# Kernel optimization log

Hardware: AMD Instinct MI355X
Metric: run time of the kernel (lower is better)

## Reference

```python
import jax, jax.numpy as jnp
import numpy as np

EPS = 1e-6
NUM_HEADS = 16
CAPACITY_FACTOR = 0.5


def _layernorm(x, g, b):
    mu = jnp.mean(x, axis=-1, keepdims=True)
    var = jnp.mean((x - mu) ** 2, axis=-1, keepdims=True)
    return (x - mu) * jax.lax.rsqrt(var + EPS) * g + b


def setup_inputs() -> dict:
    key = jax.random.key(0)
    ks = jax.random.split(key, 12)
    B, S, H, F = 2, 2048, 1024, 4096
    s = lambda d: 1.0 / np.sqrt(d)
    return {
        "x": jax.random.normal(ks[0], (B, S, H), jnp.float32),
        "w_router": jax.random.normal(ks[1], (1, H), jnp.float32) * s(H),
        "ln1_g": jnp.ones((H,), jnp.float32),
        "ln1_b": jnp.zeros((H,), jnp.float32),
        "wq": jax.random.normal(ks[2], (H, H), jnp.float32) * s(H),
        "wk": jax.random.normal(ks[3], (H, H), jnp.float32) * s(H),
        "wv": jax.random.normal(ks[4], (H, H), jnp.float32) * s(H),
        "wo": jax.random.normal(ks[5], (H, H), jnp.float32) * s(H),
        "ln2_g": jnp.ones((H,), jnp.float32),
        "ln2_b": jnp.zeros((H,), jnp.float32),
        "w_gate": jax.random.normal(ks[6], (F, H), jnp.float32) * s(H),
        "w_up": jax.random.normal(ks[7], (F, H), jnp.float32) * s(H),
        "w_down": jax.random.normal(ks[8], (H, F), jnp.float32) * s(F),
    }


def reference(x, w_router, ln1_g, ln1_b, wq, wk, wv, wo, ln2_g, ln2_b, w_gate, w_up, w_down):
    B, S, H = x.shape
    nh = NUM_HEADS
    hd = H // nh
    scale = hd ** -0.5

    # --- TokenRouter (training path, straight-through) ---
    router_logits = jnp.einsum("bsh,oh->bso", x, w_router)[..., 0]  # [B,S]
    capacity = int(S * CAPACITY_FACTOR)
    _, top_idx = jax.lax.top_k(router_logits, capacity)  # [B,cap]
    routing_mask = jnp.zeros((B, S), x.dtype).at[jnp.arange(B)[:, None], top_idx].set(1.0)
    probs = jax.nn.sigmoid(router_logits)
    routing_weights = (routing_mask + probs - jax.lax.stop_gradient(probs))[..., None]  # [B,S,1]

    # --- Attention sub-block ---
    residual = x
    xn = _layernorm(x, ln1_g, ln1_b)
    q = jnp.einsum("bsh,oh->bso", xn, wq).reshape(B, S, nh, hd).transpose(0, 2, 1, 3)
    k = jnp.einsum("bsh,oh->bso", xn, wk).reshape(B, S, nh, hd).transpose(0, 2, 1, 3)
    v = jnp.einsum("bsh,oh->bso", xn, wv).reshape(B, S, nh, hd).transpose(0, 2, 1, 3)
    scores = jnp.einsum("bnqd,bnkd->bnqk", q, k) * scale
    causal = jnp.triu(jnp.full((S, S), -jnp.inf, x.dtype), k=1)
    attn = jax.nn.softmax(scores + causal, axis=-1)
    out = jnp.einsum("bnqk,bnkd->bnqd", attn, v).transpose(0, 2, 1, 3).reshape(B, S, H)
    attn_out = jnp.einsum("bsh,oh->bso", out, wo)
    x = residual + routing_weights * attn_out

    # --- FFN sub-block (SwiGLU) ---
    residual = x
    xn = _layernorm(x, ln2_g, ln2_b)
    gate = jax.nn.silu(jnp.einsum("bsh,fh->bsf", xn, w_gate))
    up = jnp.einsum("bsh,fh->bsf", xn, w_up)
    ffn_out = jnp.einsum("bsf,hf->bsh", gate * up, w_down)
    x = residual + routing_weights * ffn_out

    return x, router_logits
```

## Files before the change

### kernel.cpp

```cpp
#include <hip/hip_runtime.h>
#include <hip/hip_bf16.h>

typedef unsigned short u16;
typedef __attribute__((ext_vector_type(4))) float f32x4;
typedef __attribute__((ext_vector_type(8))) short short8;
typedef __attribute__((ext_vector_type(4))) unsigned short ushort4v;

#define LOG2E 1.4426950408889634f

__device__ __forceinline__ u16 f2bfu(float f) {
  unsigned int u = __float_as_uint(f);
  u += 0x7FFFu + ((u >> 16) & 1u);
  return (u16)(u >> 16);
}
__device__ __forceinline__ f32x4 mfma16(short8 a, short8 b, f32x4 c) {
  return __builtin_amdgcn_mfma_f32_16x16x32_bf16(a, b, c, 0, 0, 0);
}
__device__ __forceinline__ void gld16(const void* g, void* l) {
  __builtin_amdgcn_global_load_lds(
      (const __attribute__((address_space(1))) void*)g,
      (__attribute__((address_space(3))) void*)l, 16, 0, 0);
}
template <int CTRL>
__device__ __forceinline__ float dppf(float x) {
  int xi = __float_as_int(x);
  return __int_as_float(__builtin_amdgcn_update_dpp(xi, xi, CTRL, 0xf, 0xf, false));
}
__device__ __forceinline__ float rsum16(float v) {
  v += dppf<0x121>(v);
  v += dppf<0x122>(v);
  v += dppf<0x124>(v);
  v += dppf<0x128>(v);
  return v;
}

__global__ void k_cvt7(const float* __restrict__ s0, const float* __restrict__ s1,
                       const float* __restrict__ s2, const float* __restrict__ s3,
                       const float* __restrict__ s4, const float* __restrict__ s5,
                       const float* __restrict__ s6,
                       u16* __restrict__ d0, u16* __restrict__ d1, u16* __restrict__ d2,
                       u16* __restrict__ d3, u16* __restrict__ d4, u16* __restrict__ d5,
                       u16* __restrict__ d6) {
  const int y = blockIdx.y;
  const float* src; u16* dst; int n4;
  switch (y) {
    case 0: src = s0; dst = d0; n4 = 262144; break;
    case 1: src = s1; dst = d1; n4 = 262144; break;
    case 2: src = s2; dst = d2; n4 = 262144; break;
    case 3: src = s3; dst = d3; n4 = 262144; break;
    case 4: src = s4; dst = d4; n4 = 1048576; break;
    case 5: src = s5; dst = d5; n4 = 1048576; break;
    default: src = s6; dst = d6; n4 = 1048576; break;
  }
  int i = blockIdx.x * blockDim.x + threadIdx.x;
  if (i < n4) {
    float4 v = ((const float4*)src)[i];
    ushort4v o;
    o.x = f2bfu(v.x); o.y = f2bfu(v.y); o.z = f2bfu(v.z); o.w = f2bfu(v.w);
    *(ushort4v*)(dst + (size_t)i * 4) = o;
  }
}

__global__ void k_router_ln(const float* __restrict__ x, const float* __restrict__ wr,
                            const float* __restrict__ g, const float* __restrict__ bb,
                            float* __restrict__ logits, float* __restrict__ out_lg,
                            float* __restrict__ out_x, u16* __restrict__ xn) {
  int t = blockIdx.x * 4 + (threadIdx.x >> 6);
  int l = threadIdx.x & 63;
  const float* xp = x + (size_t)t * 1024;
  float* op = out_x + (size_t)t * 1024;
  float4 xv[4];
  float s = 0.f, sq = 0.f, lg = 0.f;
#pragma unroll
  for (int p = 0; p < 4; ++p) {
    xv[p] = *(const float4*)(xp + (p * 64 + l) * 4);
    float4 wv = *(const float4*)(wr + (p * 64 + l) * 4);
    lg += xv[p].x * wv.x + xv[p].y * wv.y + xv[p].z * wv.z + xv[p].w * wv.w;
    s += xv[p].x + xv[p].y + xv[p].z + xv[p].w;
    sq += xv[p].x * xv[p].x + xv[p].y * xv[p].y + xv[p].z * xv[p].z + xv[p].w * xv[p].w;
    *(float4*)(op + (p * 64 + l) * 4) = xv[p];
  }
#pragma unroll
  for (int off = 32; off; off >>= 1) {
    lg += __shfl_xor(lg, off);
    s += __shfl_xor(s, off);
    sq += __shfl_xor(sq, off);
  }
  float mu = s * (1.f / 1024.f);
  float var = sq * (1.f / 1024.f) - mu * mu;
  float rs = rsqrtf(var + 1e-6f);
#pragma unroll
  for (int p = 0; p < 4; ++p) {
    float4 gv = *(const float4*)(g + (p * 64 + l) * 4);
    float4 bv = *(const float4*)(bb + (p * 64 + l) * 4);
    ushort4v o;
    o.x = f2bfu((xv[p].x - mu) * rs * gv.x + bv.x);
    o.y = f2bfu((xv[p].y - mu) * rs * gv.y + bv.y);
    o.z = f2bfu((xv[p].z - mu) * rs * gv.z + bv.z);
    o.w = f2bfu((xv[p].w - mu) * rs * gv.w + bv.w);
    *(ushort4v*)(xn + (size_t)t * 1024 + (p * 64 + l) * 4) = o;
  }
  if (l == 0) { logits[t] = lg; out_lg[t] = lg; }
}

__global__ void k_mask(const float* __restrict__ logits, float* __restrict__ mask) {
  __shared__ float lg[2048];
  int b = blockIdx.y;
  const float* lp = logits + b * 2048;
  for (int j = threadIdx.x; j < 2048; j += 256) lg[j] = lp[j];
  __syncthreads();
  int t = threadIdx.x >> 2, qtr = threadIdx.x & 3;
  int i = blockIdx.x * 64 + t;
  float my = lg[i];
  int cnt = 0;
  for (int j = qtr * 512; j < qtr * 512 + 512; j += 4) {
    float4 v = *(const float4*)&lg[j];
    cnt += (v.x > my) || (v.x == my && (j + 0) < i);
    cnt += (v.y > my) || (v.y == my && (j + 1) < i);
    cnt += (v.z > my) || (v.z == my && (j + 2) < i);
    cnt += (v.w > my) || (v.w == my && (j + 3) < i);
  }
  cnt += __shfl_xor(cnt, 1);
  cnt += __shfl_xor(cnt, 2);
  if (qtr == 0) mask[b * 2048 + i] = (cnt < 1024) ? 1.0f : 0.0f;
}

__global__ void k_scan(const float* __restrict__ mask, int* __restrict__ idx) {
  __shared__ int wsum[4];
  int b = blockIdx.x;
  const float* mp = mask + b * 2048;
  int t = threadIdx.x, lane = t & 63, wv = t >> 6;
  int sel[8]; int c = 0;
#pragma unroll
  for (int j = 0; j < 8; ++j) { sel[j] = mp[t * 8 + j] > 0.5f; c += sel[j]; }
  int sc = c;
#pragma unroll
  for (int off = 1; off < 64; off <<= 1) {
    int u = __shfl_up(sc, off);
    if (lane >= off) sc += u;
  }
  if (lane == 63) wsum[wv] = sc;
  __syncthreads();
  int woff = 0;
  for (int i = 0; i < wv; ++i) woff += wsum[i];
  int pos = woff + sc - c;
#pragma unroll
  for (int j = 0; j < 8; ++j)
    if (sel[j]) idx[b * 1024 + pos++] = t * 8 + j;
}

__global__ void k_vtrans(const u16* __restrict__ V, u16* __restrict__ VT) {
  int bh = blockIdx.y;
  int b = bh >> 4, h = bh & 15;
  int w = threadIdx.x >> 6, l = threadIdx.x & 63;
  int s0 = (blockIdx.x * 4 + w) * 32;
  const u16* vb = V + ((size_t)b * 2048) * 1024 + h * 64 + l;
  u16 vals[32];
#pragma unroll
  for (int j = 0; j < 32; ++j) vals[j] = vb[(size_t)(s0 + j) * 1024];
  u16* ob = VT + ((size_t)bh * 64 + l) * 2048 + s0;
#pragma unroll
  for (int c = 0; c < 4; ++c) {
    short8 o;
#pragma unroll
    for (int j = 0; j < 8; ++j) o[j] = (short)vals[c * 8 + j];
    *(short8*)&ob[c * 8] = o;
  }
}

__device__ __forceinline__ void gemm_core64(
    const u16* __restrict__ A, const u16* __restrict__ W,
    u16 (&Al)[2][128][64], u16 (&Bl)[2][128][64],
    int m0, int n0, int K, int k0, int nsteps, f32x4 (&acc)[4][4]) {
  const int tid = threadIdx.x, w = tid >> 6, l = tid & 63;
  const int wr = (w >> 1) * 64, wc = (w & 1) * 64;
#pragma unroll
  for (int mt = 0; mt < 4; ++mt)
#pragma unroll
    for (int nt = 0; nt < 4; ++nt) acc[mt][nt] = (f32x4){0.f, 0.f, 0.f, 0.f};

  auto stage = [&](int bf, int t) {
#pragma unroll
    for (int i = 0; i < 4; ++i) {
      const int bc = (i * 4 + w) * 64;
      const int chunk = bc + l;
      const int row = chunk >> 3, cc = chunk & 7;
      gld16(A + (size_t)(m0 + row) * K + k0 + t * 64 + cc * 8, (char*)(&Al[bf][0][0]) + bc * 16);
      gld16(W + (size_t)(n0 + row) * K + k0 + t * 64 + cc * 8, (char*)(&Bl[bf][0][0]) + bc * 16);
    }
  };

  stage(0, 0);
  for (int t = 0; t < nsteps; ++t) {
    __syncthreads();
    if (t + 1 < nsteps) stage((t + 1) & 1, t + 1);
    const int bf = t & 1;
#pragma unroll
    for (int kk = 0; kk < 2; ++kk) {
      const int ko = kk * 32 + (l >> 4) * 8;
      short8 af[4], bv[4];
#pragma unroll
      for (int mt = 0; mt < 4; ++mt) af[mt] = *(const short8*)&Al[bf][wr + mt * 16 + (l & 15)][ko];
#pragma unroll
      for (int nt = 0; nt < 4; ++nt) bv[nt] = *(const short8*)&Bl[bf][wc + nt * 16 + (l & 15)][ko];
#pragma unroll
      for (int mt = 0; mt < 4; ++mt)
#pragma unroll
        for (int nt = 0; nt < 4; ++nt)
          acc[mt][nt] = mfma16(af[mt], bv[nt], acc[mt][nt]);
    }
  }
}

__global__ __launch_bounds__(256, 3)
void k_qkv2(const u16* __restrict__ A, const int* __restrict__ idx,
            const u16* __restrict__ Wq, const u16* __restrict__ Wk, const u16* __restrict__ Wv,
            u16* __restrict__ Qc, u16* __restrict__ Ko, u16* __restrict__ Vo) {
  __shared__ alignas(16) u16 Al[2][128][32];
  __shared__ alignas(16) u16 Bl[2][128][32];
  const int tid = threadIdx.x, w = tid >> 6, l = tid & 63;
  const int b = blockIdx.x, xcd = b & 7, j = b >> 3;
  const u16* W; u16* Ot; int m0, n0; bool isQ;
  if (j < 16) {
    isQ = true;
    int rowg = (xcd >> 1) * 4 + (j >> 2);
    int col  = (xcd & 1) * 4 + (j & 3);
    m0 = rowg * 128; n0 = col * 128; W = Wq; Ot = Qc;
  } else {
    isQ = false;
    int jj = j - 16;
    int rowg = (xcd >> 1) * 8 + (jj >> 3);
    int colg = (xcd & 1) * 8 + (jj & 7);
    m0 = rowg * 128; n0 = (colg & 7) * 128;
    W = (colg >> 3) ? Wv : Wk; Ot = (colg >> 3) ? Vo : Ko;
  }
  int srow[2];
#pragma unroll
  for (int i = 0; i < 2; ++i) {
    int r = (i * 256 + tid) >> 2;
    int row = m0 + r;
    if (isQ) {
      int b2 = row >> 10;
      srow[i] = b2 * 2048 + idx[b2 * 1024 + (row & 1023)];
    } else srow[i] = row;
  }
  const int wr = (w >> 1) * 64, wc = (w & 1) * 64;
  f32x4 acc[4][4];
#pragma unroll
  for (int mt = 0; mt < 4; ++mt)
#pragma unroll
    for (int nt = 0; nt < 4; ++nt) acc[mt][nt] = (f32x4){0.f, 0.f, 0.f, 0.f};

  auto stage = [&](int bf, int t) {
#pragma unroll
    for (int i = 0; i < 2; ++i) {
      const int c = i * 256 + tid;
      const int r = c >> 2, cc = c & 3;
      gld16(A + (size_t)srow[i] * 1024 + t * 32 + cc * 8, (char*)(&Al[bf][0][0]) + c * 16);
      gld16(W + (size_t)(n0 + r) * 1024 + t * 32 + cc * 8, (char*)(&Bl[bf][0][0]) + c * 16);
    }
  };

  stage(0, 0);
  for (int t = 0; t < 32; ++t) {
    __syncthreads();
    if (t + 1 < 32) stage((t + 1) & 1, t + 1);
    const int bf = t & 1;
    const int ko = (l >> 4) * 8;
    short8 af[4], bv[4];
#pragma unroll
    for (int mt = 0; mt < 4; ++mt) af[mt] = *(const short8*)&Al[bf][wr + mt * 16 + (l & 15)][ko];
#pragma unroll
    for (int nt = 0; nt < 4; ++nt) bv[nt] = *(const short8*)&Bl[bf][wc + nt * 16 + (l & 15)][ko];
#pragma unroll
    for (int mt = 0; mt < 4; ++mt)
#pragma unroll
      for (int nt = 0; nt < 4; ++nt)
        acc[mt][nt] = mfma16(af[mt], bv[nt], acc[mt][nt]);
  }
#pragma unroll
  for (int mt = 0; mt < 4; ++mt)
#pragma unroll
    for (int nt = 0; nt < 4; ++nt) {
      int row = m0 + wr + mt * 16 + ((l >> 4) << 2);
      int colo = n0 + wc + nt * 16 + (l & 15);
#pragma unroll
      for (int r = 0; r < 4; ++r)
        Ot[(size_t)(row + r) * 1024 + colo] = f2bfu(acc[mt][nt][r]);
    }
}

__global__ __launch_bounds__(256, 2)
void k_projsk(const u16* __restrict__ A, const u16* __restrict__ W,
              float* __restrict__ P0, float* __restrict__ P1,
              float* __restrict__ P2, float* __restrict__ P3,
              int K, int slice) {
  __shared__ alignas(16) u16 Al[2][128][64];
  __shared__ alignas(16) u16 Bl[2][128][64];
  const int b = blockIdx.x, xcd = b & 7, k = b >> 3;
  const int pair = xcd * 8 + (k >> 3);
  const int rowg = pair >> 2, z = pair & 3, col = k & 7;
  const int n0 = col * 128, m0 = rowg * 128, k0 = z * slice;
  float* P = z == 0 ? P0 : (z == 1 ? P1 : (z == 2 ? P2 : P3));
  f32x4 acc[4][4];
  gemm_core64(A, W, Al, Bl, m0, n0, K, k0, slice >> 6, acc);
  const int tid = threadIdx.x, w = tid >> 6, l = tid & 63;
  const int wr = (w >> 1) * 64, wc = (w & 1) * 64;
#pragma unroll
  for (int mt = 0; mt < 4; ++mt)
#pragma unroll
    for (int nt = 0; nt < 4; ++nt) {
      int row = m0 + wr + mt * 16 + ((l >> 4) << 2);
      int colo = n0 + wc + nt * 16 + (l & 15);
#pragma unroll
      for (int r = 0; r < 4; ++r)
        P[(size_t)(row + r) * 1024 + colo] = acc[mt][nt][r];
    }
}

__global__ void k_combine(const float* __restrict__ P0, const float* __restrict__ P1,
                          const float* __restrict__ P2, const float* __restrict__ P3,
                          const int* __restrict__ idx, const float* __restrict__ resid,
                          float* __restrict__ out) {
  int slot = blockIdx.x * 2 + (threadIdx.x >> 7);
  int c0 = (threadIdx.x & 127) * 8;
  int b = slot >> 10;
  int orig = idx[b * 1024 + (slot & 1023)];
  size_t po = (size_t)slot * 1024 + c0;
  size_t go = ((size_t)(b * 2048 + orig)) * 1024 + c0;
#pragma unroll
  for (int h = 0; h < 2; ++h) {
    float4 a = *(const float4*)(P0 + po + h * 4);
    float4 bb = *(const float4*)(P1 + po + h * 4);
    float4 c = *(const float4*)(P2 + po + h * 4);
    float4 d = *(const float4*)(P3 + po + h * 4);
    float4 rr = *(const float4*)(resid + go + h * 4);
    float4 o;
    o.x = rr.x + a.x + bb.x + c.x + d.x;
    o.y = rr.y + a.y + bb.y + c.y + d.y;
    o.z = rr.z + a.z + bb.z + c.z + d.z;
    o.w = rr.w + a.w + bb.w + c.w + d.w;
    *(float4*)(out + go + h * 4) = o;
  }
}

__global__ void k_combine_ln(const float* __restrict__ P0, const float* __restrict__ P1,
                             const float* __restrict__ P2, const float* __restrict__ P3,
                             const int* __restrict__ idx, const float* __restrict__ resid,
                             const float* __restrict__ g, const float* __restrict__ bb,
                             float* __restrict__ out, u16* __restrict__ xn2) {
  __shared__ float red[2][2][2];
  int sh = threadIdx.x >> 7;
  int slot = blockIdx.x * 2 + sh;
  int tl = threadIdx.x & 127;
  int c0 = tl * 8;
  int b = slot >> 10;
  int orig = idx[b * 1024 + (slot & 1023)];
  size_t po = (size_t)slot * 1024 + c0;
  size_t go = ((size_t)(b * 2048 + orig)) * 1024 + c0;
  float v[8];
  float s = 0.f, sq = 0.f;
#pragma unroll
  for (int h = 0; h < 2; ++h) {
    float4 a = *(const float4*)(P0 + po + h * 4);
    float4 b4 = *(const float4*)(P1 + po + h * 4);
    float4 c = *(const float4*)(P2 + po + h * 4);
    float4 d = *(const float4*)(P3 + po + h * 4);
    float4 rr = *(const float4*)(resid + go + h * 4);
    float4 o;
    o.x = rr.x + a.x + b4.x + c.x + d.x;
    o.y = rr.y + a.y + b4.y + c.y + d.y;
    o.z = rr.z + a.z + b4.z + c.z + d.z;
    o.w = rr.w + a.w + b4.w + c.w + d.w;
    *(float4*)(out + go + h * 4) = o;
    v[h * 4 + 0] = o.x; v[h * 4 + 1] = o.y; v[h * 4 + 2] = o.z; v[h * 4 + 3] = o.w;
    s += o.x + o.y + o.z + o.w;
    sq += o.x * o.x + o.y * o.y + o.z * o.z + o.w * o.w;
  }
#pragma unroll
  for (int off = 32; off; off >>= 1) { s += __shfl_xor(s, off); sq += __shfl_xor(sq, off); }
  if ((tl & 63) == 0) { red[sh][tl >> 6][0] = s; red[sh][tl >> 6][1] = sq; }
  __syncthreads();
  float ts = red[sh][0][0] + red[sh][1][0];
  float tsq = red[sh][0][1] + red[sh][1][1];
  float mu = ts * (1.f / 1024.f);
  float var = tsq * (1.f / 1024.f) - mu * mu;
  float rs = rsqrtf(var + 1e-6f);
#pragma unroll
  for (int h = 0; h < 2; ++h) {
    float4 gv = *(const float4*)(g + c0 + h * 4);
    float4 bv = *(const float4*)(bb + c0 + h * 4);
    ushort4v o;
    o.x = f2bfu((v[h * 4 + 0] - mu) * rs * gv.x + bv.x);
    o.y = f2bfu((v[h * 4 + 1] - mu) * rs * gv.y + bv.y);
    o.z = f2bfu((v[h * 4 + 2] - mu) * rs * gv.z + bv.z);
    o.w = f2bfu((v[h * 4 + 3] - mu) * rs * gv.w + bv.w);
    *(ushort4v*)(xn2 + (size_t)slot * 1024 + c0 + h * 4) = o;
  }
}

__global__ __launch_bounds__(256, 2)
void k_ffn_dual(const u16* __restrict__ A, const u16* __restrict__ Wg, const u16* __restrict__ Wu,
                u16* __restrict__ H, int N, int K) {
  __shared__ alignas(16) u16 Al[2][128][32];
  __shared__ alignas(16) u16 Bgl[2][128][32];
  __shared__ alignas(16) u16 Bul[2][128][32];
  const int tid = threadIdx.x, w = tid >> 6, l = tid & 63;
  const int b = blockIdx.x, xcd = b & 7, k = b >> 3;
  const int rowg = (xcd >> 2) * 8 + (k >> 3);
  const int col  = (xcd & 3) * 8 + (k & 7);
  const int n0 = col * 128, m0 = rowg * 128;
  const int wr = (w >> 1) * 64, wc = (w & 1) * 64;
  f32x4 ag[4][4], au[4][4];
#pragma unroll
  for (int mt = 0; mt < 4; ++mt)
#pragma unroll
    for (int nt = 0; nt < 4; ++nt) {
      ag[mt][nt] = (f32x4){0.f, 0.f, 0.f, 0.f};
      au[mt][nt] = (f32x4){0.f, 0.f, 0.f, 0.f};
    }
  const int nsteps = K >> 5;

  auto stage = [&](int bf, int t) {
#pragma unroll
    for (int i = 0; i < 2; ++i) {
      const int bc = (i * 4 + w) * 64;
      const int chunk = bc + l;
      const int row = chunk >> 2, cc = chunk & 3;
      const size_t ao = (size_t)(m0 + row) * K + t * 32 + cc * 8;
      const size_t bo = (size_t)(n0 + row) * K + t * 32 + cc * 8;
      gld16(A + ao,  (char*)(&Al[bf][0][0])  + bc * 16);
      gld16(Wg + bo, (char*)(&Bgl[bf][0][0]) + bc * 16);
      gld16(Wu + bo, (char*)(&Bul[bf][0][0]) + bc * 16);
    }
  };

  stage(0, 0);
  for (int t = 0; t < nsteps; ++t) {
    __syncthreads();
    if (t + 1 < nsteps) stage((t + 1) & 1, t + 1);
    const int bf = t & 1;
    const int ko = (l >> 4) * 8;
    short8 af[4], bg[4], bu[4];
#pragma unroll
    for (int mt = 0; mt < 4; ++mt) af[mt] = *(const short8*)&Al[bf][wr + mt * 16 + (l & 15)][ko];
#pragma unroll
    for (int nt = 0; nt < 4; ++nt) {
      bg[nt] = *(const short8*)&Bgl[bf][wc + nt * 16 + (l & 15)][ko];
      bu[nt] = *(const short8*)&Bul[bf][wc + nt * 16 + (l & 15)][ko];
    }
#pragma unroll
    for (int mt = 0; mt < 4; ++mt)
#pragma unroll
      for (int nt = 0; nt < 4; ++nt) {
        ag[mt][nt] = mfma16(af[mt], bg[nt], ag[mt][nt]);
        au[mt][nt] = mfma16(af[mt], bu[nt], au[mt][nt]);
      }
  }
#pragma unroll
  for (int mt = 0; mt < 4; ++mt)
#pragma unroll
    for (int nt = 0; nt < 4; ++nt) {
      int row = m0 + wr + mt * 16 + ((l >> 4) << 2);
      int col2 = n0 + wc + nt * 16 + (l & 15);
#pragma unroll
      for (int r = 0; r < 4; ++r) {
        float g = ag[mt][nt][r], u = au[mt][nt][r];
        float sg = g / (1.f + __expf(-g));
        H[(size_t)(row + r) * N + col2] = f2bfu(sg * u);
      }
    }
}

__global__ __launch_bounds__(512, 2)
void k_attn(const u16* __restrict__ Q, const u16* __restrict__ K,
            const u16* __restrict__ VT, const int* __restrict__ idx,
            u16* __restrict__ O) {
  const int S = 2048, HH = 1024;
  const int px = blockIdx.x, bh = blockIdx.y;
  const int qt = (bh < 16) ? (15 - px) : px;
  const int b = bh >> 4, h = bh & 15;
  const int tid = threadIdx.x;
  const int g = tid >> 8;
  const int tg = tid & 255;
  const int w = tg >> 6;
  const int l = tid & 63;
  __shared__ alignas(16) u16 Kl[2][64][72];
  __shared__ alignas(16) u16 Vtl[2][64][72];
  __shared__ alignas(16) char un[20480];
  u16 (*Pl)[16][72] = (u16(*)[16][72])un;
  float (*cm)[64][20] = (float(*)[64][20])un;
  const size_t base = ((size_t)b * S) * HH + h * 64;
  const size_t qbase = ((size_t)b * 1024) * HH + h * 64;
  const u16* vtb = VT + ((size_t)bh * 64) * S;
  const int* ib = idx + b * 1024;

  const int r0 = tg >> 3,          cc0 = (tg & 7) * 8;
  const int r1 = (256 + tg) >> 3,  cc1 = (tg & 7) * 8;

  const int slot0 = qt * 64 + w * 16 + ((l >> 4) << 2);
  const int slotA = qt * 64 + w * 16 + (l & 15);
  int qp[4];
#pragma unroll
  for (int r = 0; r < 4; ++r) qp[r] = ib[slot0 + r];
  const int nkt = (ib[qt * 64 + 63] >> 6) + 1;
  const int hh = (nkt + 1) >> 1;
  const int kt_base = g ? hh : 0;
  const int kt_end  = g ? nkt : hh;

  short8 qf[2];
#pragma unroll
  for (int kk = 0; kk < 2; ++kk)
    qf[kk] = *(const short8*)&Q[qbase + (size_t)slotA * HH + kk * 32 + (l >> 4) * 8];

  f32x4 accO[4];
  float ls[4];
#pragma unroll
  for (int dt = 0; dt < 4; ++dt) accO[dt] = (f32x4){0.f, 0.f, 0.f, 0.f};
#pragma unroll
  for (int r = 0; r < 4; ++r) ls[r] = 0.f;

  short8 kreg0, kreg1, vreg0, vreg1;
  auto loadregs = [&](int kt) {
    kreg0 = *(const short8*)&K[base + (size_t)(kt * 64 + r0) * HH + cc0];
    kreg1 = *(const short8*)&K[base + (size_t)(kt * 64 + r1) * HH + cc1];
    vreg0 = *(const short8*)&vtb[(size_t)r0 * S + kt * 64 + cc0];
    vreg1 = *(const short8*)&vtb[(size_t)r1 * S + kt * 64 + cc1];
  };
  if (kt_base < kt_end) loadregs(kt_base);

  for (int i = 0; i < hh; ++i) {
    const int kt = kt_base + i;
    const bool valid = kt < kt_end;
    __syncthreads();
    if (valid) {
      *(short8*)&Kl[g][r0][cc0]  = kreg0;
      *(short8*)&Kl[g][r1][cc1]  = kreg1;
      *(short8*)&Vtl[g][r0][cc0] = vreg0;
      *(short8*)&Vtl[g][r1][cc1] = vreg1;
      if (kt + 1 < kt_end) loadregs(kt + 1);
    }
    __syncthreads();
    if (!valid) continue;

    float p[4][4];
    const int kcb = kt * 64 + (l & 15);
#pragma unroll
    for (int ct = 0; ct < 4; ++ct) {
      f32x4 a = (f32x4){0.f, 0.f, 0.f, 0.f};
#pragma unroll
      for (int kk = 0; kk < 2; ++kk) {
        short8 kf = *(const short8*)&Kl[g][ct * 16 + (l & 15)][kk * 32 + (l >> 4) * 8];
        a = mfma16(qf[kk], kf, a);
      }
#pragma unroll
      for (int r = 0; r < 4; ++r) {
        float v = a[r] * (0.125f * LOG2E) - 16.0f;
        if ((kcb + ct * 16) > qp[r]) v = -1e30f;
        p[ct][r] = v;
      }
    }
#pragma unroll
    for (int r = 0; r < 4; ++r) {
      float ps = 0.f;
#pragma unroll
      for (int ct = 0; ct < 4; ++ct) { float e = exp2f(p[ct][r]); p[ct][r] = e; ps += e; }
      ps = rsum16(ps);
      ls[r] += ps;
    }
#pragma unroll
    for (int ct = 0; ct < 4; ++ct)
#pragma unroll
      for (int r = 0; r < 4; ++r)
        Pl[g * 4 + w][((l >> 4) << 2) + r][ct * 16 + (l & 15)] = f2bfu(p[ct][r]);
    short8 pa[2];
#pragma unroll
    for (int kk = 0; kk < 2; ++kk)
      pa[kk] = *(const short8*)&Pl[g * 4 + w][l & 15][kk * 32 + (l >> 4) * 8];
#pragma unroll
    for (int dt = 0; dt < 4; ++dt)
#pragma unroll
      for (int kk = 0; kk < 2; ++kk) {
        short8 vf = *(const short8*)&Vtl[g][dt * 16 + (l & 15)][kk * 32 + (l >> 4) * 8];
        accO[dt] = mfma16(pa[kk], vf, accO[dt]);
      }
  }

  __syncthreads();
  if (g == 1) {
    float* dst = &cm[w][l][0];
#pragma unroll
    for (int r = 0; r < 4; ++r) dst[r] = ls[r];
#pragma unroll
    for (int dt = 0; dt < 4; ++dt)
#pragma unroll
      for (int r = 0; r < 4; ++r) dst[4 + dt * 4 + r] = accO[dt][r];
  }
  __syncthreads();
  if (g == 0) {
    const float* src = &cm[w][l][0];
#pragma unroll
    for (int r = 0; r < 4; ++r) {
      float lsf = ls[r] + src[r];
      float inv = 1.f / lsf;
#pragma unroll
      for (int dt = 0; dt < 4; ++dt) {
        float v = (accO[dt][r] + src[4 + dt * 4 + r]) * inv;
        O[((size_t)(b * 1024 + slot0 + r)) * HH + h * 64 + dt * 16 + (l & 15)] = f2bfu(v);
      }
    }
  }
}

extern "C" void kernel_launch(void* const* d_in, const int* in_sizes, int n_in,
                              void* d_out, int out_size, void* d_ws, size_t ws_size,
                              hipStream_t stream) {
  const float* x  = (const float*)d_in[0];
  const float* wr = (const float*)d_in[1];
  const float* g1 = (const float*)d_in[2];
  const float* b1 = (const float*)d_in[3];
  const float* wq = (const float*)d_in[4];
  const float* wk = (const float*)d_in[5];
  const float* wv = (const float*)d_in[6];
  const float* wo = (const float*)d_in[7];
  const float* g2 = (const float*)d_in[8];
  const float* b2 = (const float*)d_in[9];
  const float* wg = (const float*)d_in[10];
  const float* wu = (const float*)d_in[11];
  const float* wd = (const float*)d_in[12];

  float* out_x  = (float*)d_out;
  float* out_lg = out_x + (size_t)4096 * 1024;

  char* p = (char*)d_ws;
  float* mask   = (float*)p;             p += 16384;
  float* logits = (float*)p;             p += 16384;
  int*   idx    = (int*)p;               p += 16384;
  u16* wq_b = (u16*)p;                   p += (size_t)1048576 * 2;
  u16* wk_b = (u16*)p;                   p += (size_t)1048576 * 2;
  u16* wv_b = (u16*)p;                   p += (size_t)1048576 * 2;
  u16* wo_b = (u16*)p;                   p += (size_t)1048576 * 2;
  u16* wg_b = (u16*)p;                   p += (size_t)4194304 * 2;
  u16* wu_b = (u16*)p;                   p += (size_t)4194304 * 2;
  u16* wd_b = (u16*)p;                   p += (size_t)4194304 * 2;
  u16* xn   = (u16*)p;                   p += (size_t)4194304 * 2;
  u16* q_b  = (u16*)p;                   p += (size_t)4194304 * 2;
  u16* k_b  = (u16*)p;                   p += (size_t)4194304 * 2;
  u16* v_b  = (u16*)p;                   p += (size_t)4194304 * 2;
  u16* ao_b = (u16*)p;                   p += (size_t)2097152 * 2;
  u16* vt_b = (u16*)p;                   p += (size_t)4194304 * 2;
  float* pextra = (float*)p;             p += (size_t)2097152 * 4;
  u16* h_b  = q_b;

  float* oP0 = (float*)v_b;  float* oP1 = (float*)k_b;
  float* oP2 = (float*)vt_b; float* oP3 = pextra;
  u16* xn2 = xn;
  float* dP0 = (float*)v_b;  float* dP1 = (float*)vt_b;
  float* dP2 = pextra;       float* dP3 = (float*)xn;

  k_cvt7<<<dim3(4096, 7), 256, 0, stream>>>(wq, wk, wv, wo, wg, wu, wd,
                                            wq_b, wk_b, wv_b, wo_b, wg_b, wu_b, wd_b);

  k_router_ln<<<1024, 256, 0, stream>>>(x, wr, g1, b1, logits, out_lg, out_x, xn);
  k_mask<<<dim3(32, 2), 256, 0, stream>>>(logits, mask);
  k_scan<<<2, 256, 0, stream>>>(mask, idx);

  k_qkv2<<<640, 256, 0, stream>>>(xn, idx, wq_b, wk_b, wv_b, q_b, k_b, v_b);
  k_vtrans<<<dim3(16, 32), 256, 0, stream>>>(v_b, vt_b);
  k_attn<<<dim3(16, 32), 512, 0, stream>>>(q_b, k_b, vt_b, idx, ao_b);
  k_projsk<<<512, 256, 0, stream>>>(ao_b, wo_b, oP0, oP1, oP2, oP3, 1024, 256);
  k_combine_ln<<<1024, 256, 0, stream>>>(oP0, oP1, oP2, oP3, idx, x, g2, b2, out_x, xn2);

  k_ffn_dual<<<512, 256, 0, stream>>>(xn2, wg_b, wu_b, h_b, 4096, 1024);
  k_projsk<<<512, 256, 0, stream>>>(h_b, wd_b, dP0, dP1, dP2, dP3, 4096, 1024);
  k_combine<<<1024, 256, 0, stream>>>(dP0, dP1, dP2, dP3, idx, out_x, out_x);
}
```

Measured before the change: 221.4 us.

## Split FFN gate/up GEMM across separate wave groups with LDS exchange

The dual gate/up GEMM kernel now runs 512 threads per block, with four waves computing the gate tile and four computing the up tile, so each wave holds half the accumulators. After the K loop, the up waves write their results into LDS, which reuses the staging buffers, and the gate waves read them to apply SiLU and the product. This cuts register pressure per wave and raises the number of waves per CU. In exchange, each A fragment is read from LDS twice, the epilogue adds an LDS round trip with extra barriers, and half the waves sit idle while the output is written.

```diff
diff --git a/kernel.cpp b/kernel.cpp
--- a/kernel.cpp
+++ b/kernel.cpp
@@ -399,40 +399,34 @@
   }
 }
 
-__global__ __launch_bounds__(256, 2)
+__global__ __launch_bounds__(512, 2)
 void k_ffn_dual(const u16* __restrict__ A, const u16* __restrict__ Wg, const u16* __restrict__ Wu,
                 u16* __restrict__ H, int N, int K) {
-  __shared__ alignas(16) u16 Al[2][128][32];
-  __shared__ alignas(16) u16 Bgl[2][128][32];
-  __shared__ alignas(16) u16 Bul[2][128][32];
+  __shared__ alignas(16) char lds[65536];
+  u16 (*Al)[128][32]  = (u16(*)[128][32])(lds);
+  u16 (*Bgl)[128][32] = (u16(*)[128][32])(lds + 16384);
+  u16 (*Bul)[128][32] = (u16(*)[128][32])(lds + 32768);
+  float (*ex)[64]     = (float(*)[64])(lds);
   const int tid = threadIdx.x, w = tid >> 6, l = tid & 63;
   const int b = blockIdx.x, xcd = b & 7, k = b >> 3;
   const int rowg = (xcd >> 2) * 8 + (k >> 3);
   const int col  = (xcd & 3) * 8 + (k & 7);
   const int n0 = col * 128, m0 = rowg * 128;
-  const int wr = (w >> 1) * 64, wc = (w & 1) * 64;
-  f32x4 ag[4][4], au[4][4];
+  const int q = w & 3;
+  const int wr = (q >> 1) * 64, wc = (q & 1) * 64;
+  const bool isGate = w < 4;
+  f32x4 acc[4][4];
 #pragma unroll
   for (int mt = 0; mt < 4; ++mt)
 #pragma unroll
-    for (int nt = 0; nt < 4; ++nt) {
-      ag[mt][nt] = (f32x4){0.f, 0.f, 0.f, 0.f};
-      au[mt][nt] = (f32x4){0.f, 0.f, 0.f, 0.f};
-    }
+    for (int nt = 0; nt < 4; ++nt) acc[mt][nt] = (f32x4){0.f, 0.f, 0.f, 0.f};
   const int nsteps = K >> 5;
 
+  const int srow = tid >> 2, scc = tid & 3;
   auto stage = [&](int bf, int t) {
-#pragma unroll
-    for (int i = 0; i < 2; ++i) {
-      const int bc = (i * 4 + w) * 64;
-      const int chunk = bc + l;
-      const int row = chunk >> 2, cc = chunk & 3;
-      const size_t ao = (size_t)(m0 + row) * K + t * 32 + cc * 8;
-      const size_t bo = (size_t)(n0 + row) * K + t * 32 + cc * 8;
-      gld16(A + ao,  (char*)(&Al[bf][0][0])  + bc * 16);
-      gld16(Wg + bo, (char*)(&Bgl[bf][0][0]) + bc * 16);
-      gld16(Wu + bo, (char*)(&Bul[bf][0][0]) + bc * 16);
-    }
+    gld16(A  + (size_t)(m0 + srow) * K + t * 32 + scc * 8, (char*)(&Al[bf][0][0])  + tid * 16);
+    gld16(Wg + (size_t)(n0 + srow) * K + t * 32 + scc * 8, (char*)(&Bgl[bf][0][0]) + tid * 16);
+    gld16(Wu + (size_t)(n0 + srow) * K + t * 32 + scc * 8, (char*)(&Bul[bf][0][0]) + tid * 16);
   };
 
   stage(0, 0);
@@ -441,35 +435,50 @@
     if (t + 1 < nsteps) stage((t + 1) & 1, t + 1);
     const int bf = t & 1;
     const int ko = (l >> 4) * 8;
-    short8 af[4], bg[4], bu[4];
+    short8 af[4], bv[4];
 #pragma unroll
     for (int mt = 0; mt < 4; ++mt) af[mt] = *(const short8*)&Al[bf][wr + mt * 16 + (l & 15)][ko];
-#pragma unroll
-    for (int nt = 0; nt < 4; ++nt) {
-      bg[nt] = *(const short8*)&Bgl[bf][wc + nt * 16 + (l & 15)][ko];
-      bu[nt] = *(const short8*)&Bul[bf][wc + nt * 16 + (l & 15)][ko];
+    if (isGate) {
+#pragma unroll
+      for (int nt = 0; nt < 4; ++nt) bv[nt] = *(const short8*)&Bgl[bf][wc + nt * 16 + (l & 15)][ko];
+    } else {
+#pragma unroll
+      for (int nt = 0; nt < 4; ++nt) bv[nt] = *(const short8*)&Bul[bf][wc + nt * 16 + (l & 15)][ko];
     }
 #pragma unroll
     for (int mt = 0; mt < 4; ++mt)
 #pragma unroll
+      for (int nt = 0; nt < 4; ++nt)
+        acc[mt][nt] = mfma16(af[mt], bv[nt], acc[mt][nt]);
+  }
+
+  __syncthreads();
+  if (!isGate) {
+#pragma unroll
+    for (int mt = 0; mt < 4; ++mt)
+#pragma unroll
+      for (int nt = 0; nt < 4; ++nt)
+#pragma unroll
+        for (int r = 0; r < 4; ++r)
+          ex[((q * 4 + mt) * 4 + nt) * 4 + r][l] = acc[mt][nt][r];
+  }
+  __syncthreads();
+  if (isGate) {
+#pragma unroll
+    for (int mt = 0; mt < 4; ++mt)
+#pragma unroll
       for (int nt = 0; nt < 4; ++nt) {
-        ag[mt][nt] = mfma16(af[mt], bg[nt], ag[mt][nt]);
-        au[mt][nt] = mfma16(af[mt], bu[nt], au[mt][nt]);
+        int row = m0 + wr + mt * 16 + ((l >> 4) << 2);
+        int col2 = n0 + wc + nt * 16 + (l & 15);
+#pragma unroll
+        for (int r = 0; r < 4; ++r) {
+          float gv = acc[mt][nt][r];
+          float uu = ex[((q * 4 + mt) * 4 + nt) * 4 + r][l];
+          float sg = gv / (1.f + __expf(-gv));
+          H[(size_t)(row + r) * N + col2] = f2bfu(sg * uu);
+        }
       }
   }
-#pragma unroll
-  for (int mt = 0; mt < 4; ++mt)
-#pragma unroll
-    for (int nt = 0; nt < 4; ++nt) {
-      int row = m0 + wr + mt * 16 + ((l >> 4) << 2);
-      int col2 = n0 + wc + nt * 16 + (l & 15);
-#pragma unroll
-      for (int r = 0; r < 4; ++r) {
-        float g = ag[mt][nt][r], u = au[mt][nt][r];
-        float sg = g / (1.f + __expf(-g));
-        H[(size_t)(row + r) * N + col2] = f2bfu(sg * u);
-      }
-    }
 }
 
 __global__ __launch_bounds__(512, 2)
@@ -671,7 +680,7 @@
   k_projsk<<<512, 256, 0, stream>>>(ao_b, wo_b, oP0, oP1, oP2, oP3, 1024, 256);
   k_combine_ln<<<1024, 256, 0, stream>>>(oP0, oP1, oP2, oP3, idx, x, g2, b2, out_x, xn2);
 
-  k_ffn_dual<<<512, 256, 0, stream>>>(xn2, wg_b, wu_b, h_b, 4096, 1024);
+  k_ffn_dual<<<512, 512, 0, stream>>>(xn2, wg_b, wu_b, h_b, 4096, 1024);
   k_projsk<<<512, 256, 0, stream>>>(h_b, wd_b, dP0, dP1, dP2, dP3, 4096, 1024);
   k_combine<<<1024, 256, 0, stream>>>(dP0, dP1, dP2, dP3, idx, out_x, out_x);
 }
```

After: 215.9 us (median of 2 runs). -2.5%, faster.
